# Kernel tuning notes

Measured on AMD Instinct MI355X. Metric: run time of the kernel, lower is better.

The kernel has to match this reference:

```python
import jax, jax.numpy as jnp
import numpy as np

C = 4096
N = 16384


def setup_inputs() -> dict:
    key = jax.random.key(0)
    k1, k2, k3 = jax.random.split(key, 3)
    x = jax.random.normal(k1, (N, C), dtype=jnp.float32)
    # fc params, torch default init: U(-1/sqrt(C), 1/sqrt(C))
    bound = 1.0 / np.sqrt(C)
    W = jax.random.uniform(k2, (C, C), dtype=jnp.float32, minval=-bound, maxval=bound)
    b = jax.random.uniform(k3, (C,), dtype=jnp.float32, minval=-bound, maxval=bound)
    return {"x": x, "W": W, "b": b, "scale_factor": 2}


def reference(x, W, b, scale_factor):
    # MyGAP_fc: mean over batch -> [1, C] (kept as [C])
    x_gap = jnp.mean(x, axis=0)                      # [C]
    # fc: torch Linear y = x @ W.T + b
    x_scale = x_gap @ W.T + b                        # [C]
    x_scale = jax.nn.sigmoid(x_scale * scale_factor) # [C]
    # training-mode path (no hard thresholding)
    # MyScale_fc: per-channel broadcast multiply
    x_out = x * x_scale[None, :]                     # [N, C]
    return (x_out, x_scale)
```

## Files before the change

### kernel.cpp

```cpp
#include <hip/hip_runtime.h>

#define C 4096
#define NROWS 16384

__global__ void colsum_kernel(const float* __restrict__ x, float* __restrict__ gsum) {
    const int c4 = blockIdx.x * blockDim.x + threadIdx.x;
    const int rows_per = NROWS / gridDim.y;
    const int r0 = blockIdx.y * rows_per;
    const float4* xv = (const float4*)x;
    float4 acc = make_float4(0.f, 0.f, 0.f, 0.f);
    for (int r = r0; r < r0 + rows_per; ++r) {
        float4 v = xv[(size_t)r * (C / 4) + c4];
        acc.x += v.x; acc.y += v.y; acc.z += v.z; acc.w += v.w;
    }
    float* g = gsum + c4 * 4;
    atomicAdd(g + 0, acc.x);
    atomicAdd(g + 1, acc.y);
    atomicAdd(g + 2, acc.z);
    atomicAdd(g + 3, acc.w);
}

__global__ void matvec_kernel(const float* __restrict__ W,
                              const float* __restrict__ b,
                              const float* __restrict__ gsum,
                              const int* __restrict__ sf,
                              float* __restrict__ scale_out) {
    const int row = blockIdx.x;
    const int t = threadIdx.x;
    const float4* wv = (const float4*)(W + (size_t)row * C);
    const float4* gv = (const float4*)gsum;
    float acc = 0.f;
#pragma unroll
    for (int k = 0; k < 4; ++k) {
        const int j4 = t + k * 256;
        const float4 w = wv[j4];
        const float4 g = gv[j4];
        acc += w.x * g.x + w.y * g.y + w.z * g.z + w.w * g.w;
    }
#pragma unroll
    for (int off = 32; off > 0; off >>= 1) acc += __shfl_down(acc, off);
    __shared__ float red[4];
    if ((t & 63) == 0) red[t >> 6] = acc;
    __syncthreads();
    if (t == 0) {
        const float y = (red[0] + red[1] + red[2] + red[3]) * (1.0f / NROWS) + b[row];
        const float z = y * (float)sf[0];
        const float s = 1.0f / (1.0f + __expf(-z));
        scale_out[row] = s;
    }
}

__global__ void scale_kernel(const float* __restrict__ x,
                             const float* __restrict__ s,
                             float* __restrict__ out) {
    const float4* xv = (const float4*)x;
    const float4* sv = (const float4*)s;
    float4* ov = (float4*)out;
    const size_t total = (size_t)NROWS * C / 4;
    for (size_t i = (size_t)blockIdx.x * blockDim.x + threadIdx.x; i < total;
         i += (size_t)gridDim.x * blockDim.x) {
        float4 v = xv[i];
        const float4 sc = sv[i & 1023];
        v.x *= sc.x; v.y *= sc.y; v.z *= sc.z; v.w *= sc.w;
        ov[i] = v;
    }
}

extern "C" void kernel_launch(void* const* d_in, const int* in_sizes, int n_in,
                              void* d_out, int out_size, void* d_ws, size_t ws_size,
                              hipStream_t stream) {
    const float* x = (const float*)d_in[0];
    const float* W = (const float*)d_in[1];
    const float* b = (const float*)d_in[2];
    const int* sf  = (const int*)d_in[3];

    float* out = (float*)d_out;
    float* scale_tail = out + (size_t)NROWS * C;
    float* gsum = (float*)d_ws;

    hipMemsetAsync(gsum, 0, C * sizeof(float), stream);

    colsum_kernel<<<dim3(C / 1024, 256), 256, 0, stream>>>(x, gsum);
    matvec_kernel<<<C, 256, 0, stream>>>(W, b, gsum, sf, scale_tail);
    scale_kernel<<<2048, 256, 0, stream>>>(x, scale_tail, out);
}
```

Baseline: 184.1 us.

## Replace atomic colsum with two-pass reduction, reverse scale order, nontemporal W/out

Column sums now go through per-slice partials plus a separate reduce kernel, which removes the memset and the float atomics. W loads and output stores become nontemporal so they don't evict x from the last-level cache. The scale kernel walks x in reverse order so it starts with the tail rows colsum read most recently and may still be cached. This adds an extra launch and a 4 MB partial buffer of traffic.

```diff
diff --git a/kernel.cpp b/kernel.cpp
--- a/kernel.cpp
+++ b/kernel.cpp
@@ -2,22 +2,29 @@
 
 #define C 4096
 #define NROWS 16384
+#define PARTS 256
 
-__global__ void colsum_kernel(const float* __restrict__ x, float* __restrict__ gsum) {
+typedef float f32x4 __attribute__((ext_vector_type(4)));
+
+__global__ void colsum_partial(const float* __restrict__ x, float* __restrict__ part) {
     const int c4 = blockIdx.x * blockDim.x + threadIdx.x;
-    const int rows_per = NROWS / gridDim.y;
+    const int rows_per = NROWS / PARTS;
     const int r0 = blockIdx.y * rows_per;
-    const float4* xv = (const float4*)x;
-    float4 acc = make_float4(0.f, 0.f, 0.f, 0.f);
-    for (int r = r0; r < r0 + rows_per; ++r) {
-        float4 v = xv[(size_t)r * (C / 4) + c4];
-        acc.x += v.x; acc.y += v.y; acc.z += v.z; acc.w += v.w;
+    const f32x4* xv = (const f32x4*)x;
+    f32x4 acc = {0.f, 0.f, 0.f, 0.f};
+#pragma unroll 4
+    for (int r = 0; r < rows_per; ++r) {
+        acc += xv[(size_t)(r0 + r) * (C / 4) + c4];
     }
-    float* g = gsum + c4 * 4;
-    atomicAdd(g + 0, acc.x);
-    atomicAdd(g + 1, acc.y);
-    atomicAdd(g + 2, acc.z);
-    atomicAdd(g + 3, acc.w);
+    ((f32x4*)part)[(size_t)blockIdx.y * (C / 4) + c4] = acc;
+}
+
+__global__ void colsum_reduce(const float* __restrict__ part, float* __restrict__ gsum) {
+    const int c = blockIdx.x * blockDim.x + threadIdx.x;
+    float s = 0.f;
+#pragma unroll 8
+    for (int r = 0; r < PARTS; ++r) s += part[(size_t)r * C + c];
+    gsum[c] = s;
 }
 
 __global__ void matvec_kernel(const float* __restrict__ W,
@@ -27,14 +34,14 @@
                               float* __restrict__ scale_out) {
     const int row = blockIdx.x;
     const int t = threadIdx.x;
-    const float4* wv = (const float4*)(W + (size_t)row * C);
-    const float4* gv = (const float4*)gsum;
+    const f32x4* wv = (const f32x4*)(W + (size_t)row * C);
+    const f32x4* gv = (const f32x4*)gsum;
     float acc = 0.f;
 #pragma unroll
     for (int k = 0; k < 4; ++k) {
         const int j4 = t + k * 256;
-        const float4 w = wv[j4];
-        const float4 g = gv[j4];
+        const f32x4 w = __builtin_nontemporal_load(wv + j4);
+        const f32x4 g = gv[j4];
         acc += w.x * g.x + w.y * g.y + w.z * g.z + w.w * g.w;
     }
 #pragma unroll
@@ -53,16 +60,17 @@
 __global__ void scale_kernel(const float* __restrict__ x,
                              const float* __restrict__ s,
                              float* __restrict__ out) {
-    const float4* xv = (const float4*)x;
-    const float4* sv = (const float4*)s;
-    float4* ov = (float4*)out;
-    const size_t total = (size_t)NROWS * C / 4;
-    for (size_t i = (size_t)blockIdx.x * blockDim.x + threadIdx.x; i < total;
-         i += (size_t)gridDim.x * blockDim.x) {
-        float4 v = xv[i];
-        const float4 sc = sv[i & 1023];
-        v.x *= sc.x; v.y *= sc.y; v.z *= sc.z; v.w *= sc.w;
-        ov[i] = v;
+    const f32x4* xv = (const f32x4*)x;
+    const f32x4* sv = (const f32x4*)s;
+    f32x4* ov = (f32x4*)out;
+    const int tid = threadIdx.x;
+    const long K = (long)NROWS * C / 4 / 256;
+    for (long k = K - 1 - blockIdx.x; k >= 0; k -= gridDim.x) {
+        const size_t i = (size_t)k * 256 + tid;
+        f32x4 v = xv[i];
+        const f32x4 sc = sv[i & 1023];
+        v *= sc;
+        __builtin_nontemporal_store(v, ov + i);
     }
 }
 
@@ -76,11 +84,12 @@
 
     float* out = (float*)d_out;
     float* scale_tail = out + (size_t)NROWS * C;
-    float* gsum = (float*)d_ws;
 
-    hipMemsetAsync(gsum, 0, C * sizeof(float), stream);
+    float* part = (float*)d_ws;
+    float* gsum = part + (size_t)PARTS * C;
 
-    colsum_kernel<<<dim3(C / 1024, 256), 256, 0, stream>>>(x, gsum);
+    colsum_partial<<<dim3(C / 1024, PARTS), 256, 0, stream>>>(x, part);
+    colsum_reduce<<<C / 256, 256, 0, stream>>>(part, gsum);
     matvec_kernel<<<C, 256, 0, stream>>>(W, b, gsum, sf, scale_tail);
     scale_kernel<<<2048, 256, 0, stream>>>(x, scale_tail, out);
 }
```

After: 159.0 us. 1.16x faster.
